# Kernel optimization log

Hardware: AMD Instinct MI355X
Metric: run time of the kernel (lower is better)

Reference implementation:

```python
import jax, jax.numpy as jnp
import numpy as np

BST_DEPTH = 6
NB_SPLIT = 2**BST_DEPTH - 1          # 63 internal (split) nodes
NB_NODES = 2**(BST_DEPTH + 1) - 1    # 127 total nodes (heap layout)
SPLIT = np.arange(NB_SPLIT)
DESC_L = 2 * SPLIT + 1               # left children of split nodes
DESC_R = 2 * SPLIT + 2               # right children of split nodes


def setup_inputs() -> dict:
    key = jax.random.key(0)
    kx, ka = jax.random.split(key)
    x = jax.random.normal(kx, (131072, 512), dtype=jnp.float32)
    A = jax.random.uniform(ka, (NB_SPLIT, 512), dtype=jnp.float32)  # torch.rand init
    return {"x": x, "A": A}


def _compute_q(x, A):
    # XA[:, t] is the split score of internal node t; XA == XA[:, split_nodes]
    XA = x @ A.T                                         # [N, nb_split]
    q = jnp.ones((x.shape[0], NB_NODES), dtype=XA.dtype)  # [N, nb_nodes]
    # Seed children of each split node. NOTE: sequential semantics matter —
    # the right-child write reads q[:, SPLIT] AFTER the left-child write
    # (odd-indexed split nodes were just updated), matching torch in-place ops.
    q = q.at[:, DESC_L].set(jnp.minimum(q[:, SPLIT], XA))
    q = q.at[:, DESC_R].set(jnp.minimum(q[:, SPLIT], -XA))
    # Propagate the running min from parents down the tree, one sweep per level.
    for _ in range(BST_DEPTH):
        q = q.at[:, DESC_L].set(jnp.minimum(q[:, DESC_L], q[:, SPLIT]))
        q = q.at[:, DESC_R].set(jnp.minimum(q[:, DESC_R], q[:, SPLIT]))
    return q


def reference(x, A):
    q = _compute_q(x, A)
    z = jnp.clip(q, 0.0, 1.0)  # pruned=False: no QP pruning branch
    return z
```

## Files before the change

kernel.cpp:

```cpp
#include <hip/hip_runtime.h>
#include <hip/hip_bf16.h>
#include <cstdint>

#define KD 512
#define BM 64
#define NT 256
#define NSPLIT 63
#define NNODES 127

typedef __attribute__((ext_vector_type(8))) short bf16x8;
typedef __attribute__((ext_vector_type(4))) float f32x4;

#define MFMA_B16(a, b, c) __builtin_amdgcn_mfma_f32_16x16x32_bf16(a, b, c, 0, 0, 0)

static __device__ __forceinline__ unsigned short f2bf(float f) {
    return __builtin_bit_cast(unsigned short, __float2bfloat16(f));
}
static __device__ __forceinline__ float bf2f(unsigned short h) {
    return __builtin_bit_cast(float, (unsigned)h << 16);
}
static __device__ __forceinline__ unsigned pack2(float f0, float f1) {
    return (unsigned)f2bf(f0) | ((unsigned)f2bf(f1) << 16);
}

static __device__ __forceinline__ void cvt8(f32x4 a, f32x4 b, bf16x8& hi, bf16x8& lo) {
    const unsigned short h0 = f2bf(a[0]), h1 = f2bf(a[1]), h2 = f2bf(a[2]), h3 = f2bf(a[3]);
    const unsigned short h4 = f2bf(b[0]), h5 = f2bf(b[1]), h6 = f2bf(b[2]), h7 = f2bf(b[3]);
    uint4 H = make_uint4((unsigned)h0 | ((unsigned)h1 << 16), (unsigned)h2 | ((unsigned)h3 << 16),
                         (unsigned)h4 | ((unsigned)h5 << 16), (unsigned)h6 | ((unsigned)h7 << 16));
    uint4 L = make_uint4(pack2(a[0] - bf2f(h0), a[1] - bf2f(h1)),
                         pack2(a[2] - bf2f(h2), a[3] - bf2f(h3)),
                         pack2(b[0] - bf2f(h4), b[1] - bf2f(h5)),
                         pack2(b[2] - bf2f(h6), b[3] - bf2f(h7)));
    hi = __builtin_bit_cast(bf16x8, H);
    lo = __builtin_bit_cast(bf16x8, L);
}

static __device__ __forceinline__ void gload_lds16(const float* g, void* l) {
    __builtin_amdgcn_global_load_lds(
        (const __attribute__((address_space(1))) unsigned int*)g,
        (__attribute__((address_space(3))) unsigned int*)l, 16, 0, 0);
}

template<int N> static __device__ __forceinline__ void vmwait() {
    if constexpr (N == 2) asm volatile("s_waitcnt vmcnt(2)" ::: "memory");
    else                  asm volatile("s_waitcnt vmcnt(0)" ::: "memory");
}

template<int T>
static __device__ __forceinline__ void tree_walk(float qt, const float* __restrict__ srow,
                                                 float* __restrict__ zrow, int part) {
    const float s  = srow[T];
    const float ql = fminf(qt, s);
    const float qr = fminf(qt, -s);
    if (((2 * T + 1) >> 5) == part) zrow[2 * T + 1] = fminf(fmaxf(ql, 0.f), 1.f);
    if (((2 * T + 2) >> 5) == part) zrow[2 * T + 2] = fminf(fmaxf(qr, 0.f), 1.f);
    if constexpr (2 * T + 1 < NSPLIT) tree_walk<2 * T + 1>(ql, srow, zrow, part);
    if constexpr (2 * T + 2 < NSPLIT) tree_walk<2 * T + 2>(qr, srow, zrow, part);
}

static __device__ __forceinline__ void write_B(unsigned char* ldsb, int wb_off,
                                               bool bvalid, f32x4 b0, f32x4 b1) {
    if (!bvalid) { b0 = (f32x4)(0.f); b1 = (f32x4)(0.f); }
    bf16x8 hi, lo;
    cvt8(b0, b1, hi, lo);
    *reinterpret_cast<bf16x8*>(ldsb + 8192 + wb_off)  = hi;
    *reinterpret_cast<bf16x8*>(ldsb + 12288 + wb_off) = lo;
}

struct Ctx {
    const float* xsrc;
    const float* ag;
    unsigned char* xbf;
    unsigned char* ldsb;
    int va_off;
    int bo;
    int wb_off;
    bool bvalid;
};

template<int T>
static __device__ __forceinline__ void tiles(const Ctx& c, f32x4 (&acc)[4],
                                             f32x4& bn0, f32x4& bn1) {
    vmwait<(T == 15) ? 0 : 2>();
    __builtin_amdgcn_sched_barrier(0);
    f32x4 va = *reinterpret_cast<const f32x4*>(c.xbf + c.va_off);
    f32x4 vb = *reinterpret_cast<const f32x4*>(c.xbf + (c.va_off ^ 16));
    asm volatile("s_waitcnt lgkmcnt(0)" ::: "memory");
    __builtin_amdgcn_sched_barrier(0);
    if constexpr (T + 1 < 16) {
        gload_lds16(c.xsrc + (T + 1) * 32, c.xbf);
        gload_lds16(c.xsrc + (T + 1) * 32 + 8 * KD, c.xbf + 1024);
    }
    __builtin_amdgcn_sched_barrier(0);

    bf16x8 ah, al;
    cvt8(va, vb, ah, al);
    const unsigned char* bh = c.ldsb + 8192 + c.bo;
#pragma unroll
    for (int nf = 0; nf < 4; ++nf) {
        const bf16x8 bhv = *reinterpret_cast<const bf16x8*>(bh + nf * 1024);
        const bf16x8 blv = *reinterpret_cast<const bf16x8*>(bh + 4096 + nf * 1024);
        acc[nf] = MFMA_B16(ah, bhv, acc[nf]);
        acc[nf] = MFMA_B16(al, bhv, acc[nf]);
        acc[nf] = MFMA_B16(ah, blv, acc[nf]);
    }

    if constexpr (T + 1 < 16) {
        __builtin_amdgcn_sched_barrier(0);
        __builtin_amdgcn_s_barrier();
        write_B(c.ldsb, c.wb_off, c.bvalid, bn0, bn1);
        asm volatile("s_waitcnt lgkmcnt(0)" ::: "memory");
        __builtin_amdgcn_s_barrier();
        __builtin_amdgcn_sched_barrier(0);
        if constexpr (T + 2 < 16) {
            if (c.bvalid) {
                bn0 = *reinterpret_cast<const f32x4*>(c.ag + (T + 2) * 32);
                bn1 = *reinterpret_cast<const f32x4*>(c.ag + (T + 2) * 32 + 4);
            }
        }
        tiles<T + 1>(c, acc, bn0, bn1);
    }
}

__global__ __launch_bounds__(NT, 8)
void lt_mfma7(const float* __restrict__ x, const float* __restrict__ A,
              float* __restrict__ out) {
    __shared__ __align__(16) unsigned char lds[16384];

    const int tid  = threadIdx.x;
    const int wave = tid >> 6;
    const int lane = tid & 63;
    const int fr   = lane & 15;
    const int g    = lane >> 4;
    const int r0   = blockIdx.x * BM;

    Ctx c;
    c.ldsb  = lds;
    c.xbf   = lds + wave * 2048;
    c.xsrc  = x + (size_t)(r0 + wave * 16 + (lane >> 3)) * KD
                + (((lane & 7) ^ (lane >> 3)) << 2);
    const int brow = tid >> 2;
    const int q    = tid & 3;
    c.ag     = A + (size_t)brow * KD + q * 8;
    c.bvalid = brow < NSPLIT;
    c.wb_off = (brow << 6) + ((q ^ (brow & 3)) << 4);
    c.va_off = (fr << 7) + (((g << 1) ^ (fr & 7)) << 4);
    c.bo     = (fr << 6) + ((g ^ (fr & 3)) << 4);

    f32x4 acc[4];
#pragma unroll
    for (int j = 0; j < 4; ++j) acc[j] = (f32x4)(0.f);

    f32x4 bn0 = (f32x4)(0.f), bn1 = (f32x4)(0.f);
    if (c.bvalid) {
        bn0 = *reinterpret_cast<const f32x4*>(c.ag);
        bn1 = *reinterpret_cast<const f32x4*>(c.ag + 4);
    }
    gload_lds16(c.xsrc, c.xbf);
    gload_lds16(c.xsrc + 8 * KD, c.xbf + 1024);
    write_B(c.ldsb, c.wb_off, c.bvalid, bn0, bn1);
    asm volatile("s_waitcnt lgkmcnt(0)" ::: "memory");
    __builtin_amdgcn_s_barrier();
    if (c.bvalid) {
        bn0 = *reinterpret_cast<const f32x4*>(c.ag + 32);
        bn1 = *reinterpret_cast<const f32x4*>(c.ag + 36);
    }

    tiles<0>(c, acc, bn0, bn1);

    __syncthreads();

    float* warea = reinterpret_cast<float*>(lds);
    float* zw    = warea + 1040;
    const int o    = lane >> 2;
    const int part = lane & 3;

#pragma unroll
    for (int ph = 0; ph < 4; ++ph) {
        if (wave == ph) {
#pragma unroll
            for (int nf = 0; nf < 4; ++nf)
#pragma unroll
                for (int rg = 0; rg < 4; ++rg)
                    warea[(4 * g + rg) * 65 + nf * 16 + fr] = acc[nf][rg];
            const float* srow = warea + o * 65;
            float* zrow = zw + o * NNODES;
            if (part == 0) zrow[0] = 1.f;
            tree_walk<0>(1.f, srow, zrow, part);

            float* og = out + (size_t)(r0 + wave * 16) * NNODES;
#pragma unroll
            for (int j = 0; j < 8; ++j) {
                const int idx = j * 64 + lane;
                if (idx < 508)
                    *reinterpret_cast<f32x4*>(og + idx * 4) =
                        *reinterpret_cast<const f32x4*>(zw + idx * 4);
            }
        }
        __syncthreads();
    }
}

extern "C" void kernel_launch(void* const* d_in, const int* in_sizes, int n_in,
                              void* d_out, int out_size, void* d_ws, size_t ws_size,
                              hipStream_t stream) {
    const float* x = (const float*)d_in[0];
    const float* A = (const float*)d_in[1];
    float* out = (float*)d_out;
    const int nrows = in_sizes[0] / KD;
    const int grid = nrows / BM;
    lt_mfma7<<<dim3(grid), dim3(NT), 0, stream>>>(x, A, out);
}
```

Baseline: 83.92 us.

## Precompute bf16 hi/lo A in workspace, triple-buffer x, drop block barriers

A separate prep kernel converts A into bf16 hi/lo split planes in the workspace once per call. Each wave then reads B fragments straight from global memory (L2-resident) instead of cooperatively converting and staging them in LDS behind two block barriers per k-step. The x tile staging becomes a per-wave triple buffer with two tiles of prefetch, so waves run independently without __syncthreads. The epilogue is now per-wave in two 8-row halves instead of serialized across waves. The cost is a second kernel launch, more LDS per block (lower occupancy bound), and repeated global B loads per wave.

```diff
diff --git a/kernel.cpp b/kernel.cpp
--- a/kernel.cpp
+++ b/kernel.cpp
@@ -12,6 +12,7 @@
 typedef __attribute__((ext_vector_type(4))) float f32x4;
 
 #define MFMA_B16(a, b, c) __builtin_amdgcn_mfma_f32_16x16x32_bf16(a, b, c, 0, 0, 0)
+#define SCHED_FENCE() __builtin_amdgcn_sched_barrier(0)
 
 static __device__ __forceinline__ unsigned short f2bf(float f) {
     return __builtin_bit_cast(unsigned short, __float2bfloat16(f));
@@ -43,90 +44,91 @@
 }
 
 template<int N> static __device__ __forceinline__ void vmwait() {
-    if constexpr (N == 2) asm volatile("s_waitcnt vmcnt(2)" ::: "memory");
-    else                  asm volatile("s_waitcnt vmcnt(0)" ::: "memory");
+    if constexpr (N == 10)     asm volatile("s_waitcnt vmcnt(10)" ::: "memory");
+    else if constexpr (N == 2) asm volatile("s_waitcnt vmcnt(2)" ::: "memory");
+    else                       asm volatile("s_waitcnt vmcnt(0)" ::: "memory");
 }
 
 template<int T>
-static __device__ __forceinline__ void tree_walk(float qt, const float* __restrict__ srow,
-                                                 float* __restrict__ zrow, int part) {
+static __device__ __forceinline__ void tree_walk8(float qt, const float* __restrict__ srow,
+                                                  float* __restrict__ zrow, int part8) {
     const float s  = srow[T];
     const float ql = fminf(qt, s);
     const float qr = fminf(qt, -s);
-    if (((2 * T + 1) >> 5) == part) zrow[2 * T + 1] = fminf(fmaxf(ql, 0.f), 1.f);
-    if (((2 * T + 2) >> 5) == part) zrow[2 * T + 2] = fminf(fmaxf(qr, 0.f), 1.f);
-    if constexpr (2 * T + 1 < NSPLIT) tree_walk<2 * T + 1>(ql, srow, zrow, part);
-    if constexpr (2 * T + 2 < NSPLIT) tree_walk<2 * T + 2>(qr, srow, zrow, part);
+    if (((2 * T + 1) >> 4) == part8) zrow[2 * T + 1] = fminf(fmaxf(ql, 0.f), 1.f);
+    if (((2 * T + 2) >> 4) == part8) zrow[2 * T + 2] = fminf(fmaxf(qr, 0.f), 1.f);
+    if constexpr (2 * T + 1 < NSPLIT) tree_walk8<2 * T + 1>(ql, srow, zrow, part8);
+    if constexpr (2 * T + 2 < NSPLIT) tree_walk8<2 * T + 2>(qr, srow, zrow, part8);
 }
 
-static __device__ __forceinline__ void write_B(unsigned char* ldsb, int wb_off,
-                                               bool bvalid, f32x4 b0, f32x4 b1) {
-    if (!bvalid) { b0 = (f32x4)(0.f); b1 = (f32x4)(0.f); }
-    bf16x8 hi, lo;
-    cvt8(b0, b1, hi, lo);
-    *reinterpret_cast<bf16x8*>(ldsb + 8192 + wb_off)  = hi;
-    *reinterpret_cast<bf16x8*>(ldsb + 12288 + wb_off) = lo;
+__global__ __launch_bounds__(256)
+void lt_prep(const float* __restrict__ A, unsigned short* __restrict__ ws) {
+    const int gid = blockIdx.x * 256 + threadIdx.x;
+    const int row = gid >> 7;
+    const int c4  = (gid & 127) << 2;
+    f32x4 v = (f32x4)(0.f);
+    if (row < NSPLIT)
+        v = *reinterpret_cast<const f32x4*>(A + (size_t)row * KD + c4);
+    const unsigned short h0 = f2bf(v[0]), h1 = f2bf(v[1]), h2 = f2bf(v[2]), h3 = f2bf(v[3]);
+    uint2 hv = make_uint2((unsigned)h0 | ((unsigned)h1 << 16),
+                          (unsigned)h2 | ((unsigned)h3 << 16));
+    uint2 lv = make_uint2(pack2(v[0] - bf2f(h0), v[1] - bf2f(h1)),
+                          pack2(v[2] - bf2f(h2), v[3] - bf2f(h3)));
+    *reinterpret_cast<uint2*>(ws + row * KD + c4)         = hv;
+    *reinterpret_cast<uint2*>(ws + 32768 + row * KD + c4) = lv;
 }
 
-struct Ctx {
-    const float* xsrc;
-    const float* ag;
-    unsigned char* xbf;
-    unsigned char* ldsb;
-    int va_off;
-    int bo;
-    int wb_off;
-    bool bvalid;
-};
-
 template<int T>
-static __device__ __forceinline__ void tiles(const Ctx& c, f32x4 (&acc)[4],
-                                             f32x4& bn0, f32x4& bn1) {
-    vmwait<(T == 15) ? 0 : 2>();
-    __builtin_amdgcn_sched_barrier(0);
-    f32x4 va = *reinterpret_cast<const f32x4*>(c.xbf + c.va_off);
-    f32x4 vb = *reinterpret_cast<const f32x4*>(c.xbf + (c.va_off ^ 16));
-    asm volatile("s_waitcnt lgkmcnt(0)" ::: "memory");
-    __builtin_amdgcn_sched_barrier(0);
-    if constexpr (T + 1 < 16) {
-        gload_lds16(c.xsrc + (T + 1) * 32, c.xbf);
-        gload_lds16(c.xsrc + (T + 1) * 32 + 8 * KD, c.xbf + 1024);
+static __device__ __forceinline__ void tiles(
+        const float* xsrc, unsigned char* xw, const unsigned short* bwsl,
+        int va_off, f32x4 (&acc)[4]) {
+    const unsigned short* bp = bwsl + T * 32;
+    bf16x8 bh0 = *reinterpret_cast<const bf16x8*>(bp);
+    bf16x8 bh1 = *reinterpret_cast<const bf16x8*>(bp + 8192);
+    bf16x8 bh2 = *reinterpret_cast<const bf16x8*>(bp + 16384);
+    bf16x8 bh3 = *reinterpret_cast<const bf16x8*>(bp + 24576);
+    bf16x8 bl0 = *reinterpret_cast<const bf16x8*>(bp + 32768);
+    bf16x8 bl1 = *reinterpret_cast<const bf16x8*>(bp + 40960);
+    bf16x8 bl2 = *reinterpret_cast<const bf16x8*>(bp + 49152);
+    bf16x8 bl3 = *reinterpret_cast<const bf16x8*>(bp + 57344);
+    SCHED_FENCE();
+    if constexpr (T == 0) vmwait<10>();
+    const unsigned char* xbf = xw + (T % 3) * 2048;
+    f32x4 va = *reinterpret_cast<const f32x4*>(xbf + va_off);
+    f32x4 vb = *reinterpret_cast<const f32x4*>(xbf + (va_off ^ 16));
+    SCHED_FENCE();
+    if constexpr (T + 2 < 16) {
+        unsigned char* nb = xw + ((T + 2) % 3) * 2048;
+        gload_lds16(xsrc + (T + 2) * 32, nb);
+        gload_lds16(xsrc + (T + 2) * 32 + 4096, nb + 1024);
     }
-    __builtin_amdgcn_sched_barrier(0);
+    SCHED_FENCE();
+    vmwait<(T + 2 < 16) ? 2 : 0>();
+    SCHED_FENCE();
 
     bf16x8 ah, al;
     cvt8(va, vb, ah, al);
-    const unsigned char* bh = c.ldsb + 8192 + c.bo;
-#pragma unroll
-    for (int nf = 0; nf < 4; ++nf) {
-        const bf16x8 bhv = *reinterpret_cast<const bf16x8*>(bh + nf * 1024);
-        const bf16x8 blv = *reinterpret_cast<const bf16x8*>(bh + 4096 + nf * 1024);
-        acc[nf] = MFMA_B16(ah, bhv, acc[nf]);
-        acc[nf] = MFMA_B16(al, bhv, acc[nf]);
-        acc[nf] = MFMA_B16(ah, blv, acc[nf]);
-    }
+    acc[0] = MFMA_B16(ah, bh0, acc[0]);
+    acc[1] = MFMA_B16(ah, bh1, acc[1]);
+    acc[2] = MFMA_B16(ah, bh2, acc[2]);
+    acc[3] = MFMA_B16(ah, bh3, acc[3]);
+    acc[0] = MFMA_B16(al, bh0, acc[0]);
+    acc[1] = MFMA_B16(al, bh1, acc[1]);
+    acc[2] = MFMA_B16(al, bh2, acc[2]);
+    acc[3] = MFMA_B16(al, bh3, acc[3]);
+    acc[0] = MFMA_B16(ah, bl0, acc[0]);
+    acc[1] = MFMA_B16(ah, bl1, acc[1]);
+    acc[2] = MFMA_B16(ah, bl2, acc[2]);
+    acc[3] = MFMA_B16(ah, bl3, acc[3]);
 
-    if constexpr (T + 1 < 16) {
-        __builtin_amdgcn_sched_barrier(0);
-        __builtin_amdgcn_s_barrier();
-        write_B(c.ldsb, c.wb_off, c.bvalid, bn0, bn1);
-        asm volatile("s_waitcnt lgkmcnt(0)" ::: "memory");
-        __builtin_amdgcn_s_barrier();
-        __builtin_amdgcn_sched_barrier(0);
-        if constexpr (T + 2 < 16) {
-            if (c.bvalid) {
-                bn0 = *reinterpret_cast<const f32x4*>(c.ag + (T + 2) * 32);
-                bn1 = *reinterpret_cast<const f32x4*>(c.ag + (T + 2) * 32 + 4);
-            }
-        }
-        tiles<T + 1>(c, acc, bn0, bn1);
-    }
+    if constexpr (T + 1 < 16)
+        tiles<T + 1>(xsrc, xw, bwsl, va_off, acc);
 }
 
-__global__ __launch_bounds__(NT, 8)
-void lt_mfma7(const float* __restrict__ x, const float* __restrict__ A,
+__global__ __launch_bounds__(NT, 6)
+void lt_mfma8(const float* __restrict__ x, const unsigned short* __restrict__ bws,
               float* __restrict__ out) {
-    __shared__ __align__(16) unsigned char lds[16384];
+    __shared__ __align__(16) unsigned char lds[24576];
 
     const int tid  = threadIdx.x;
     const int wave = tid >> 6;
@@ -135,70 +137,51 @@
     const int g    = lane >> 4;
     const int r0   = blockIdx.x * BM;
 
-    Ctx c;
-    c.ldsb  = lds;
-    c.xbf   = lds + wave * 2048;
-    c.xsrc  = x + (size_t)(r0 + wave * 16 + (lane >> 3)) * KD
-                + (((lane & 7) ^ (lane >> 3)) << 2);
-    const int brow = tid >> 2;
-    const int q    = tid & 3;
-    c.ag     = A + (size_t)brow * KD + q * 8;
-    c.bvalid = brow < NSPLIT;
-    c.wb_off = (brow << 6) + ((q ^ (brow & 3)) << 4);
-    c.va_off = (fr << 7) + (((g << 1) ^ (fr & 7)) << 4);
-    c.bo     = (fr << 6) + ((g ^ (fr & 3)) << 4);
+    unsigned char* xw = lds + wave * 6144;
+    const float* xsrc = x + (size_t)(r0 + wave * 16 + (lane >> 3)) * KD
+                          + (((lane & 7) ^ ((lane >> 3) & 7)) << 2);
+    const unsigned short* bwsl = bws + fr * KD + g * 8;
+    const int va_off = (fr << 7) + (((g << 1) ^ (fr & 7)) << 4);
 
     f32x4 acc[4];
 #pragma unroll
     for (int j = 0; j < 4; ++j) acc[j] = (f32x4)(0.f);
 
-    f32x4 bn0 = (f32x4)(0.f), bn1 = (f32x4)(0.f);
-    if (c.bvalid) {
-        bn0 = *reinterpret_cast<const f32x4*>(c.ag);
-        bn1 = *reinterpret_cast<const f32x4*>(c.ag + 4);
-    }
-    gload_lds16(c.xsrc, c.xbf);
-    gload_lds16(c.xsrc + 8 * KD, c.xbf + 1024);
-    write_B(c.ldsb, c.wb_off, c.bvalid, bn0, bn1);
-    asm volatile("s_waitcnt lgkmcnt(0)" ::: "memory");
-    __builtin_amdgcn_s_barrier();
-    if (c.bvalid) {
-        bn0 = *reinterpret_cast<const f32x4*>(c.ag + 32);
-        bn1 = *reinterpret_cast<const f32x4*>(c.ag + 36);
-    }
+    gload_lds16(xsrc, xw);
+    gload_lds16(xsrc + 4096, xw + 1024);
+    gload_lds16(xsrc + 32, xw + 2048);
+    gload_lds16(xsrc + 32 + 4096, xw + 3072);
+    SCHED_FENCE();
 
-    tiles<0>(c, acc, bn0, bn1);
+    tiles<0>(xsrc, xw, bwsl, va_off, acc);
 
-    __syncthreads();
-
-    float* warea = reinterpret_cast<float*>(lds);
-    float* zw    = warea + 1040;
-    const int o    = lane >> 2;
-    const int part = lane & 3;
+    float* warea = reinterpret_cast<float*>(xw);
+    float* zw    = warea + 520;
+    const int o  = lane >> 3;
+    const int p8 = lane & 7;
 
 #pragma unroll
-    for (int ph = 0; ph < 4; ++ph) {
-        if (wave == ph) {
+    for (int s = 0; s < 2; ++s) {
+        if ((g >> 1) == s) {
 #pragma unroll
             for (int nf = 0; nf < 4; ++nf)
 #pragma unroll
                 for (int rg = 0; rg < 4; ++rg)
-                    warea[(4 * g + rg) * 65 + nf * 16 + fr] = acc[nf][rg];
-            const float* srow = warea + o * 65;
-            float* zrow = zw + o * NNODES;
-            if (part == 0) zrow[0] = 1.f;
-            tree_walk<0>(1.f, srow, zrow, part);
+                    warea[((g & 1) * 4 + rg) * 65 + nf * 16 + fr] = acc[nf][rg];
+        }
+        const float* srow = warea + o * 65;
+        float* zrow = zw + o * NNODES;
+        if (p8 == 0) zrow[0] = 1.f;
+        tree_walk8<0>(1.f, srow, zrow, p8);
 
-            float* og = out + (size_t)(r0 + wave * 16) * NNODES;
+        float* og = out + (size_t)(r0 + wave * 16 + s * 8) * NNODES;
 #pragma unroll
-            for (int j = 0; j < 8; ++j) {
-                const int idx = j * 64 + lane;
-                if (idx < 508)
-                    *reinterpret_cast<f32x4*>(og + idx * 4) =
-                        *reinterpret_cast<const f32x4*>(zw + idx * 4);
-            }
+        for (int j = 0; j < 4; ++j) {
+            const int idx = j * 64 + lane;
+            if (idx < 254)
+                *reinterpret_cast<f32x4*>(og + idx * 4) =
+                    *reinterpret_cast<const f32x4*>(zw + idx * 4);
         }
-        __syncthreads();
     }
 }
 
@@ -208,7 +191,8 @@
     const float* x = (const float*)d_in[0];
     const float* A = (const float*)d_in[1];
     float* out = (float*)d_out;
+    unsigned short* ws = (unsigned short*)d_ws;
     const int nrows = in_sizes[0] / KD;
-    const int grid = nrows / BM;
-    lt_mfma7<<<dim3(grid), dim3(NT), 0, stream>>>(x, A, out);
+    lt_prep<<<dim3(32), dim3(256), 0, stream>>>(A, ws);
+    lt_mfma8<<<dim3(nrows / BM), dim3(NT), 0, stream>>>(x, ws, out);
 }
```

After: 225.1 us. 168% more time.
